# Optimization experiments

Measured on AMD Instinct MI355X. Metric: run time of the kernel, lower is better.

## Reference

```python
import jax, jax.numpy as jnp
import numpy as np

C = 512
G = 32  # num_norm_groups
EPS = 1e-6


def setup_inputs() -> dict:
    key = jax.random.key(0)
    ks = jax.random.split(key, 10)
    B, H, W = 8, 64, 64
    s = 1.0 / np.sqrt(C)
    return {
        "x": jax.random.normal(ks[0], (B, C, H, W), dtype=jnp.float32),
        "gamma": jnp.ones((C,), jnp.float32),
        "beta": jnp.zeros((C,), jnp.float32),
        "Wq": jax.random.uniform(ks[1], (C, C), jnp.float32, -s, s),
        "bq": jax.random.uniform(ks[2], (C,), jnp.float32, -s, s),
        "Wk": jax.random.uniform(ks[3], (C, C), jnp.float32, -s, s),
        "bk": jax.random.uniform(ks[4], (C,), jnp.float32, -s, s),
        "Wv": jax.random.uniform(ks[5], (C, C), jnp.float32, -s, s),
        "bv": jax.random.uniform(ks[6], (C,), jnp.float32, -s, s),
        "Wo": jax.random.uniform(ks[7], (C, C), jnp.float32, -s, s),
    }


def group_norm(x, gamma, beta):
    # x: [B, C, H, W]; normalize over each group of C//G channels and all spatial dims
    B, Cc, H, W = x.shape
    xg = x.reshape(B, G, Cc // G, H, W)
    mean = jnp.mean(xg, axis=(2, 3, 4), keepdims=True)
    var = jnp.var(xg, axis=(2, 3, 4), keepdims=True)
    xg = (xg - mean) * jax.lax.rsqrt(var + EPS)
    x = xg.reshape(B, Cc, H, W)
    return x * gamma[None, :, None, None] + beta[None, :, None, None]


def reference(x, gamma, beta, Wq, bq, Wk, bk, Wv, bv, Wo):
    B, Cc, H, W = x.shape
    out = group_norm(x, gamma, beta)
    # [B, C, H, W] -> [B, H*W, C]
    out = out.transpose(0, 2, 3, 1).reshape(B, H * W, Cc)
    q = out @ Wq.T + bq
    k = out @ Wk.T + bk
    v = out @ Wv.T + bv
    score = jnp.einsum('bic,bjc->bij', q, k) / jnp.sqrt(jnp.float32(Cc))
    score = jax.nn.softmax(score, axis=-1)
    out = jnp.einsum('bij,bjc->bic', score, v)
    out = out @ Wo.T
    out = out.reshape(B, H, W, Cc).transpose(0, 3, 1, 2)
    return out + x
```

## Files before the change

### kernel.cpp

```cpp
#include <hip/hip_runtime.h>
#include <hip/hip_bf16.h>
#include <cstdint>
#include <cstddef>

typedef __hip_bfloat16 BF;
typedef __attribute__((ext_vector_type(8))) short bhalf8;
typedef __attribute__((ext_vector_type(4))) float floatx4;

#define NB 8
#define NC 512
#define NHW 4096
#define NG 32

__device__ __forceinline__ float b2f(short h) {
    union { unsigned u; float f; } c;
    c.u = ((unsigned)(unsigned short)h) << 16;
    return c.f;
}
__device__ __forceinline__ short f2b(float f) {
    __hip_bfloat16 h = __float2bfloat16(f);
    short s;
    __builtin_memcpy(&s, &h, 2);
    return s;
}

__device__ __forceinline__ void gload16(const BF* g, BF* l) {
    __builtin_amdgcn_global_load_lds(
        (const __attribute__((address_space(1))) void*)g,
        (__attribute__((address_space(3))) void*)l, 16, 0, 0);
}

__device__ __forceinline__ void xcd_swizzle(int& bx, int& by) {
    const int gx = gridDim.x;
    const int nwg = gx * gridDim.y;
    if ((nwg & 7) == 0) {
        const int lin = by * gx + bx;
        const int cpx = nwg >> 3;
        const int s = (lin & 7) * cpx + (lin >> 3);
        bx = s % gx;
        by = s / gx;
    }
}

__global__ __launch_bounds__(256) void f2b_convert4(const float* __restrict__ s0,
                                                    const float* __restrict__ s1,
                                                    const float* __restrict__ s2,
                                                    const float* __restrict__ s3,
                                                    BF* __restrict__ dst) {
    const int which = blockIdx.x >> 8;
    const float* src = (which == 0) ? s0 : (which == 1) ? s1 : (which == 2) ? s2 : s3;
    BF* d = dst + (long)which * (NC * NC);
    const int i = ((blockIdx.x & 255) * 256 + threadIdx.x) * 4;
    float4 v = *(const float4*)&src[i];
    d[i]     = __float2bfloat16(v.x);
    d[i + 1] = __float2bfloat16(v.y);
    d[i + 2] = __float2bfloat16(v.z);
    d[i + 3] = __float2bfloat16(v.w);
}

__global__ __launch_bounds__(256) void gn_stats(const float* __restrict__ x,
                                                float* __restrict__ stats) {
    const int bg = blockIdx.x;
    const long base = (long)bg * 65536;
    float s = 0.f, q = 0.f;
    for (int i = threadIdx.x * 4; i < 65536; i += 256 * 4) {
        float4 v4 = *(const float4*)&x[base + i];
        s += v4.x + v4.y + v4.z + v4.w;
        q += v4.x * v4.x + v4.y * v4.y + v4.z * v4.z + v4.w * v4.w;
    }
#pragma unroll
    for (int o = 32; o; o >>= 1) { s += __shfl_down(s, o); q += __shfl_down(q, o); }
    __shared__ float rs[4], rq[4];
    const int w = threadIdx.x >> 6;
    if ((threadIdx.x & 63) == 0) { rs[w] = s; rq[w] = q; }
    __syncthreads();
    if (threadIdx.x == 0) {
        s = rs[0] + rs[1] + rs[2] + rs[3];
        q = rq[0] + rq[1] + rq[2] + rq[3];
        float mean = s * (1.f / 65536.f);
        float var = q * (1.f / 65536.f) - mean * mean;
        stats[2 * bg]     = mean;
        stats[2 * bg + 1] = rsqrtf(fmaxf(var, 0.f) + 1e-6f);
    }
}

__global__ __launch_bounds__(256) void gn_apply(const float* __restrict__ x,
                                                const float* __restrict__ gamma,
                                                const float* __restrict__ beta,
                                                const float* __restrict__ stats,
                                                BF* __restrict__ n) {
    __shared__ float tile[64][65];
    const int b = blockIdx.z, c0 = blockIdx.y * 64, s0 = blockIdx.x * 64;
    const long xbase = ((long)b * NC + c0) * NHW + s0;
#pragma unroll
    for (int i = 0; i < 16; i++) {
        int lin = i * 256 + threadIdx.x;
        int cl = lin >> 6, sl = lin & 63;
        int c = c0 + cl;
        float2 mr = ((const float2*)stats)[b * NG + (c >> 4)];
        float v = x[xbase + (long)cl * NHW + sl];
        v = (v - mr.x) * mr.y * gamma[c] + beta[c];
        tile[cl][sl] = v;
    }
    __syncthreads();
    const long nbase = ((long)b * NHW + s0) * NC + c0;
#pragma unroll
    for (int i = 0; i < 16; i++) {
        int lin = i * 256 + threadIdx.x;
        int sl = lin >> 6, cl = lin & 63;
        n[nbase + (long)sl * NC + cl] = __float2bfloat16(tile[cl][sl]);
    }
}

template <bool BIAS, bool TRANS, bool RESID>
__global__ __launch_bounds__(256, 2) void gemm128(
    const BF* __restrict__ A, long aStride,
    const BF* __restrict__ Bm, long bStride,
    BF* __restrict__ C, long cStride,
    const float* __restrict__ bias,
    const float* __restrict__ resid, float* __restrict__ outF,
    int M, int N, int K, float scale)
{
    __shared__ __align__(16) BF sA[128 * 32];
    __shared__ __align__(16) BF sB[128 * 32];
    const int tid = threadIdx.x;
    const int wave = tid >> 6, lane = tid & 63;
    int bxi = blockIdx.x, byi = blockIdx.y;
    xcd_swizzle(bxi, byi);
    const int bm = byi * 128, bn = bxi * 128;
    const BF* Ab = A + (long)blockIdx.z * aStride + (long)bm * K;
    const BF* Bb = Bm + (long)blockIdx.z * bStride + (long)bn * K;

    const int srow = wave * 32 + (lane >> 2);
    const int sk = (lane & 3) * 8;
    const BF* gA0 = Ab + (long)srow * K + sk;
    const BF* gA1 = gA0 + (long)16 * K;
    const BF* gB0 = Bb + (long)srow * K + sk;
    const BF* gB1 = gB0 + (long)16 * K;
    BF* lA0 = &sA[(wave * 32) * 32];
    BF* lA1 = &sA[(wave * 32 + 16) * 32];
    BF* lB0 = &sB[(wave * 32) * 32];
    BF* lB1 = &sB[(wave * 32 + 16) * 32];

    floatx4 acc[4][4];
#pragma unroll
    for (int i = 0; i < 4; i++)
#pragma unroll
        for (int j = 0; j < 4; j++) acc[i][j] = (floatx4){0.f, 0.f, 0.f, 0.f};

    const int wm = (wave >> 1) * 64, wn = (wave & 1) * 64;
    const int lr = lane & 15, lk = (lane >> 4) * 8;

    for (int k0 = 0; k0 < K; k0 += 32) {
        __syncthreads();
        gload16(gA0 + k0, lA0);
        gload16(gA1 + k0, lA1);
        gload16(gB0 + k0, lB0);
        gload16(gB1 + k0, lB1);
        __syncthreads();
        bhalf8 af[4], bfr[4];
#pragma unroll
        for (int i = 0; i < 4; i++)
            af[i] = *(const bhalf8*)&sA[(wm + i * 16 + lr) * 32 + lk];
#pragma unroll
        for (int i = 0; i < 4; i++)
            bfr[i] = *(const bhalf8*)&sB[(wn + i * 16 + lr) * 32 + lk];
#pragma unroll
        for (int mi = 0; mi < 4; mi++)
#pragma unroll
            for (int ni = 0; ni < 4; ni++)
                acc[mi][ni] = __builtin_amdgcn_mfma_f32_16x16x32_bf16(
                    af[mi], bfr[ni], acc[mi][ni], 0, 0, 0);
    }

    if (RESID) {
        float* Ob = outF + (long)blockIdx.z * cStride;
        const float* Xb = resid + (long)blockIdx.z * cStride;
#pragma unroll
        for (int ni = 0; ni < 4; ni++) {
            const int col = bn + wn + ni * 16 + lr;
#pragma unroll
            for (int mi = 0; mi < 4; mi++) {
                const int row0 = bm + wm + mi * 16 + (lane >> 4) * 4;
                const long a = (long)col * M + row0;
                float4 xv = *(const float4*)&Xb[a];
                float4 ov;
                ov.x = acc[mi][ni][0] * scale + xv.x;
                ov.y = acc[mi][ni][1] * scale + xv.y;
                ov.z = acc[mi][ni][2] * scale + xv.z;
                ov.w = acc[mi][ni][3] * scale + xv.w;
                *(float4*)&Ob[a] = ov;
            }
        }
        return;
    }

    BF* Cb = C + (long)blockIdx.z * cStride;
#pragma unroll
    for (int ni = 0; ni < 4; ni++) {
        const int col = bn + wn + ni * 16 + lr;
        const float bv = BIAS ? bias[col] : 0.0f;
#pragma unroll
        for (int mi = 0; mi < 4; mi++) {
            const int row0 = bm + wm + mi * 16 + (lane >> 4) * 4;
#pragma unroll
            for (int r = 0; r < 4; r++) {
                float v = acc[mi][ni][r] * scale + bv;
                if (TRANS) Cb[(long)col * M + row0 + r] = __float2bfloat16(v);
                else       Cb[(long)(row0 + r) * N + col] = __float2bfloat16(v);
            }
        }
    }
}

__global__ __launch_bounds__(256, 2) void gemm64(
    const BF* __restrict__ A, long aStride,
    const BF* __restrict__ Bm, long bStride,
    BF* __restrict__ C, long cStride,
    int N, int K, float scale)
{
    __shared__ __align__(16) BF sA[64 * 32];
    __shared__ __align__(16) BF sB[128 * 32];
    const int tid = threadIdx.x;
    const int wave = tid >> 6, lane = tid & 63;
    int bxi = blockIdx.x, byi = blockIdx.y;
    xcd_swizzle(bxi, byi);
    const int bm = byi * 64, bn = bxi * 128;
    const BF* Ab = A + (long)blockIdx.z * aStride + (long)bm * K;
    const BF* Bb = Bm + (long)blockIdx.z * bStride + (long)bn * K;

    const int rowoff = lane >> 2, sk = (lane & 3) * 8;
    const BF* gA0 = Ab + (long)(wave * 16 + rowoff) * K + sk;
    const BF* gB0 = Bb + (long)(wave * 32 + rowoff) * K + sk;
    const BF* gB1 = gB0 + (long)16 * K;
    BF* lA0 = &sA[(wave * 16) * 32];
    BF* lB0 = &sB[(wave * 32) * 32];
    BF* lB1 = &sB[(wave * 32 + 16) * 32];

    floatx4 acc[2][4];
#pragma unroll
    for (int i = 0; i < 2; i++)
#pragma unroll
        for (int j = 0; j < 4; j++) acc[i][j] = (floatx4){0.f, 0.f, 0.f, 0.f};

    const int wm = (wave >> 1) * 32, wn = (wave & 1) * 64;
    const int lr = lane & 15, lk = (lane >> 4) * 8;

    for (int k0 = 0; k0 < K; k0 += 32) {
        __syncthreads();
        gload16(gA0 + k0, lA0);
        gload16(gB0 + k0, lB0);
        gload16(gB1 + k0, lB1);
        __syncthreads();
        bhalf8 af[2], bfr[4];
#pragma unroll
        for (int i = 0; i < 2; i++)
            af[i] = *(const bhalf8*)&sA[(wm + i * 16 + lr) * 32 + lk];
#pragma unroll
        for (int i = 0; i < 4; i++)
            bfr[i] = *(const bhalf8*)&sB[(wn + i * 16 + lr) * 32 + lk];
#pragma unroll
        for (int mi = 0; mi < 2; mi++)
#pragma unroll
            for (int ni = 0; ni < 4; ni++)
                acc[mi][ni] = __builtin_amdgcn_mfma_f32_16x16x32_bf16(
                    af[mi], bfr[ni], acc[mi][ni], 0, 0, 0);
    }

    BF* Cb = C + (long)blockIdx.z * cStride;
#pragma unroll
    for (int ni = 0; ni < 4; ni++) {
        const int col = bn + wn + ni * 16 + lr;
#pragma unroll
        for (int mi = 0; mi < 2; mi++) {
            const int row0 = bm + wm + mi * 16 + (lane >> 4) * 4;
#pragma unroll
            for (int r = 0; r < 4; r++)
                Cb[(long)(row0 + r) * N + col] = __float2bfloat16(acc[mi][ni][r] * scale);
        }
    }
}

__global__ __launch_bounds__(256) void softmax4096(BF* __restrict__ S) {
    const long base = (long)blockIdx.x * 4096 + threadIdx.x * 16;
    const int tid = threadIdx.x, w = tid >> 6;
    bhalf8 u = *(bhalf8*)&S[base];
    bhalf8 u2 = *(bhalf8*)&S[base + 8];
    float v[16];
    float m = -1e30f;
#pragma unroll
    for (int j = 0; j < 8; j++) { v[j] = b2f(u[j]); v[8 + j] = b2f(u2[j]); }
#pragma unroll
    for (int j = 0; j < 16; j++) m = fmaxf(m, v[j]);
#pragma unroll
    for (int o = 32; o; o >>= 1) m = fmaxf(m, __shfl_xor(m, o));
    __shared__ float rm[4], rs[4];
    if ((tid & 63) == 0) rm[w] = m;
    __syncthreads();
    m = fmaxf(fmaxf(rm[0], rm[1]), fmaxf(rm[2], rm[3]));
    float s = 0.f;
#pragma unroll
    for (int j = 0; j < 16; j++) { v[j] = __expf(v[j] - m); s += v[j]; }
#pragma unroll
    for (int o = 32; o; o >>= 1) s += __shfl_xor(s, o);
    if ((tid & 63) == 0) rs[w] = s;
    __syncthreads();
    s = rs[0] + rs[1] + rs[2] + rs[3];
    const float inv = 1.0f / s;
#pragma unroll
    for (int j = 0; j < 8; j++) { u[j] = f2b(v[j] * inv); u2[j] = f2b(v[8 + j] * inv); }
    *(bhalf8*)&S[base] = u;
    *(bhalf8*)&S[base + 8] = u2;
}

extern "C" void kernel_launch(void* const* d_in, const int* in_sizes, int n_in,
                              void* d_out, int out_size, void* d_ws, size_t ws_size,
                              hipStream_t stream) {
    const float* x     = (const float*)d_in[0];
    const float* gamma = (const float*)d_in[1];
    const float* beta  = (const float*)d_in[2];
    const float* Wq    = (const float*)d_in[3];
    const float* bq    = (const float*)d_in[4];
    const float* Wk    = (const float*)d_in[5];
    const float* bk    = (const float*)d_in[6];
    const float* Wv    = (const float*)d_in[7];
    const float* bv    = (const float*)d_in[8];
    const float* Wo    = (const float*)d_in[9];
    float* out = (float*)d_out;

    const long ACTB = (long)NHW * NC;
    const long SB   = (long)NHW * NHW;
    const long WSZ  = (long)NC * NC;

    char* ws = (char*)d_ws;
    float* stats = (float*)ws;
    BF* wb = (BF*)(ws + 4096);
    BF* q  = wb + 4 * WSZ;
    BF* kk = q + NB * ACTB;
    BF* vT = kk + NB * ACTB;
    BF* R  = vT + NB * ACTB;
    BF* n = R;
    BF* S = R;

    const size_t base_need = 4096ull + (size_t)4 * WSZ * 2 + (size_t)3 * NB * ACTB * 2;
    long sroom = (ws_size > base_need) ? (long)((ws_size - base_need) / (SB * 2)) : 1;
    int chunk = (int)(sroom < 1 ? 1 : (sroom > NB ? NB : sroom));
    while (NB % chunk) chunk--;

    f2b_convert4<<<1024, 256, 0, stream>>>(Wq, Wk, Wv, Wo, wb);

    gn_stats<<<NB * NG, 256, 0, stream>>>(x, stats);
    gn_apply<<<dim3(NHW / 64, NC / 64, NB), 256, 0, stream>>>(x, gamma, beta, stats, n);

    gemm128<true, false, false><<<dim3(NC / 128, NHW / 128, NB), 256, 0, stream>>>(
        n, ACTB, wb + 0 * WSZ, 0, q, ACTB, bq, nullptr, nullptr, NHW, NC, NC, 1.0f);
    gemm128<true, false, false><<<dim3(NC / 128, NHW / 128, NB), 256, 0, stream>>>(
        n, ACTB, wb + 1 * WSZ, 0, kk, ACTB, bk, nullptr, nullptr, NHW, NC, NC, 1.0f);
    gemm128<true, true, false><<<dim3(NC / 128, NHW / 128, NB), 256, 0, stream>>>(
        n, ACTB, wb + 2 * WSZ, 0, vT, ACTB, bv, nullptr, nullptr, NHW, NC, NC, 1.0f);

    const float iscl = 0.044194173824159216f;
    for (int b0 = 0; b0 < NB; b0 += chunk) {
        gemm128<false, false, false><<<dim3(NHW / 128, NHW / 128, chunk), 256, 0, stream>>>(
            q + b0 * ACTB, ACTB, kk + b0 * ACTB, ACTB, S, SB, nullptr, nullptr, nullptr,
            NHW, NHW, NC, iscl);
        softmax4096<<<NHW * chunk, 256, 0, stream>>>(S);
        if (chunk >= 4)
            gemm128<false, false, false><<<dim3(NC / 128, NHW / 128, chunk), 256, 0, stream>>>(
                S, SB, vT + b0 * ACTB, ACTB, q + b0 * ACTB, ACTB, nullptr, nullptr, nullptr,
                NHW, NC, NHW, 1.0f);
        else
            gemm64<<<dim3(NC / 128, NHW / 64, chunk), 256, 0, stream>>>(
                S, SB, vT + b0 * ACTB, ACTB, q + b0 * ACTB, ACTB, NC, NHW, 1.0f);
    }

    gemm128<false, true, true><<<dim3(NC / 128, NHW / 128, NB), 256, 0, stream>>>(
        q, ACTB, wb + 3 * WSZ, 0, nullptr, ACTB, nullptr, x, out, NHW, NC, NC, 1.0f);
}
```

Measured before the change: 795.4 us.

## Add 256x256 double-buffered pipelined MFMA GEMM and use it for all large GEMMs

Introduces a 512-thread gemm256 kernel with 256x256 tiles and a 64-wide K step. It double-buffers 128KB of LDS with swizzled layout, interleaves global-to-LDS staging with MFMA quadrants, and uses explicit barriers, waitcnt and s_setprio. It replaces gemm128 for the QKV projections, the QK^T score GEMM, the PV GEMM (when chunk>=4) and the output projection with residual. The goal is more data reuse per tile and hiding load latency behind MFMA work. The cost is heavy LDS use that allows only one block per CU, fewer blocks for the small-N GEMMs, and fragile hand-written synchronisation.

```diff
diff --git a/kernel.cpp b/kernel.cpp
--- a/kernel.cpp
+++ b/kernel.cpp
@@ -29,6 +29,14 @@
         (const __attribute__((address_space(1))) void*)g,
         (__attribute__((address_space(3))) void*)l, 16, 0, 0);
 }
+
+__device__ __forceinline__ void BARRIER() {
+    asm volatile("" ::: "memory");
+    __builtin_amdgcn_s_barrier();
+    asm volatile("" ::: "memory");
+}
+#define WAITVM(N) asm volatile("s_waitcnt vmcnt(" #N ")" ::: "memory")
+#define WAITLGKM() asm volatile("s_waitcnt lgkmcnt(0)" ::: "memory")
 
 __device__ __forceinline__ void xcd_swizzle(int& bx, int& by) {
     const int gx = gridDim.x;
@@ -112,13 +120,211 @@
     }
 }
 
+#define LDA8(buf, mf, ks) (*(const bhalf8*)(sL + (buf) * 65536 + aOff + (mf) * 2048 + (ks) * 64))
+#define LDB8(buf, nf, ks) (*(const bhalf8*)(sL + (buf) * 65536 + bOff + (nf) * 2048 + (ks) * 64))
+#define QUAD(M0, N0)                                                                     \
+    {                                                                                    \
+        _Pragma("unroll") for (int mf = (M0); mf < (M0) + 4; mf++)                       \
+            _Pragma("unroll") for (int nf = (N0); nf < (N0) + 2; nf++) {                 \
+            acc[mf][nf] = __builtin_amdgcn_mfma_f32_16x16x32_bf16(                       \
+                aR[mf & 3][0], bR[nf][0], acc[mf][nf], 0, 0, 0);                         \
+            acc[mf][nf] = __builtin_amdgcn_mfma_f32_16x16x32_bf16(                       \
+                aR[mf & 3][1], bR[nf][1], acc[mf][nf], 0, 0, 0);                         \
+        }                                                                                \
+    }
+
 template <bool BIAS, bool TRANS, bool RESID>
+__global__ __launch_bounds__(512) void gemm256(
+    const BF* __restrict__ A, long aStride,
+    const BF* __restrict__ Bm, long bStride,
+    BF* __restrict__ C, long cStride,
+    const float* __restrict__ bias,
+    const float* __restrict__ resid, float* __restrict__ outF,
+    int M, int N, int K, float scale)
+{
+    __shared__ __align__(16) char sL[131072];
+    const int tid = threadIdx.x;
+    const int wave = tid >> 6, lane = tid & 63;
+    int bxi = blockIdx.x, byi = blockIdx.y;
+    xcd_swizzle(bxi, byi);
+    const int bm = byi * 256, bn = bxi * 256;
+    const BF* Ab = A + (long)blockIdx.z * aStride + (long)bm * K;
+    const BF* Bb = Bm + (long)blockIdx.z * bStride + (long)bn * K;
+
+    const int d0 = tid * 16, d1 = 8192 + tid * 16;
+    const int p0 = d0 ^ (((d0 >> 9) & 1) << 5);
+    const int p1 = d1 ^ (((d1 >> 9) & 1) << 5);
+    const int soff0 = (p0 >> 7) * K + ((p0 & 127) >> 1);
+    const int soff1 = (p1 >> 7) * K + ((p1 & 127) >> 1);
+    const int lds0 = wave * 1024;
+    const int lds1 = 8192 + wave * 1024;
+
+    const int lr = lane & 15, lk2 = (lane >> 4) * 16;
+    const int sbase = (lr * 128 + lk2) ^ (((lr >> 2) & 1) << 5);
+    const int aOff = (wave >> 2) * 16384 + sbase;
+    const int bOff = (2 + ((wave >> 1) & 1)) * 16384 + (wave & 1) * 8192 + sbase;
+
+    auto STAGE = [&](int t, int region, int dbuf) {
+        const BF* g = ((region < 2) ? (Ab + (long)region * 128 * K)
+                                    : (Bb + (long)(region - 2) * 128 * K)) + (long)t * 64;
+        char* lb = sL + dbuf * 65536 + region * 16384;
+        gload16(g + soff0, (BF*)(lb + lds0));
+        gload16(g + soff1, (BF*)(lb + lds1));
+    };
+
+    floatx4 acc[8][4];
+#pragma unroll
+    for (int i = 0; i < 8; i++)
+#pragma unroll
+        for (int j = 0; j < 4; j++) acc[i][j] = (floatx4){0.f, 0.f, 0.f, 0.f};
+
+    const int nt = K >> 6, ngrp = nt >> 1;
+
+    STAGE(0, 0, 0); STAGE(0, 1, 0); STAGE(0, 2, 0); STAGE(0, 3, 0);
+    WAITVM(4);
+    STAGE(1, 2, 1); STAGE(1, 3, 1); STAGE(1, 0, 1);
+    WAITVM(6);
+    BARRIER();
+
+    bhalf8 aR[4][2], bR[4][2];
+
+    for (int g = 0; g < ngrp; ++g) {
+        const bool st = (g < ngrp - 1);
+        const int t2 = 2 * g + 2, t3 = 2 * g + 3;
+
+#pragma unroll
+        for (int mf = 0; mf < 4; mf++) { aR[mf][0] = LDA8(0, mf, 0); aR[mf][1] = LDA8(0, mf, 1); }
+#pragma unroll
+        for (int nf = 0; nf < 2; nf++) { bR[nf][0] = LDB8(0, nf, 0); bR[nf][1] = LDB8(0, nf, 1); }
+        if (!(wave & 2)) {
+#pragma unroll
+            for (int nf = 2; nf < 4; nf++) { bR[nf][0] = LDB8(0, nf, 0); bR[nf][1] = LDB8(0, nf, 1); }
+        }
+        STAGE(2 * g + 1, 1, 1);
+        BARRIER(); WAITLGKM();
+        __builtin_amdgcn_s_setprio(1);
+        QUAD(0, 0);
+        __builtin_amdgcn_s_setprio(0);
+        BARRIER();
+
+        if (wave & 2) {
+#pragma unroll
+            for (int nf = 2; nf < 4; nf++) { bR[nf][0] = LDB8(0, nf, 0); bR[nf][1] = LDB8(0, nf, 1); }
+        }
+        if (st) STAGE(t2, 2, 0);
+        BARRIER(); WAITLGKM();
+        __builtin_amdgcn_s_setprio(1);
+        QUAD(0, 2);
+        __builtin_amdgcn_s_setprio(0);
+        BARRIER();
+
+#pragma unroll
+        for (int mf = 4; mf < 8; mf++) { aR[mf & 3][0] = LDA8(0, mf, 0); aR[mf & 3][1] = LDA8(0, mf, 1); }
+        if (st) STAGE(t2, 3, 0);
+        BARRIER(); WAITLGKM();
+        __builtin_amdgcn_s_setprio(1);
+        QUAD(4, 0);
+        __builtin_amdgcn_s_setprio(0);
+        BARRIER();
+
+        if (st) STAGE(t2, 0, 0);
+        BARRIER();
+        __builtin_amdgcn_s_setprio(1);
+        QUAD(4, 2);
+        __builtin_amdgcn_s_setprio(0);
+        if (st) { WAITVM(6); } else { WAITVM(0); }
+        BARRIER();
+
+#pragma unroll
+        for (int mf = 0; mf < 4; mf++) { aR[mf][0] = LDA8(1, mf, 0); aR[mf][1] = LDA8(1, mf, 1); }
+#pragma unroll
+        for (int nf = 0; nf < 2; nf++) { bR[nf][0] = LDB8(1, nf, 0); bR[nf][1] = LDB8(1, nf, 1); }
+        if (!(wave & 2)) {
+#pragma unroll
+            for (int nf = 2; nf < 4; nf++) { bR[nf][0] = LDB8(1, nf, 0); bR[nf][1] = LDB8(1, nf, 1); }
+        }
+        if (st) STAGE(t2, 1, 0);
+        BARRIER(); WAITLGKM();
+        __builtin_amdgcn_s_setprio(1);
+        QUAD(0, 0);
+        __builtin_amdgcn_s_setprio(0);
+        BARRIER();
+
+        if (wave & 2) {
+#pragma unroll
+            for (int nf = 2; nf < 4; nf++) { bR[nf][0] = LDB8(1, nf, 0); bR[nf][1] = LDB8(1, nf, 1); }
+        }
+        if (st) STAGE(t3, 2, 1);
+        BARRIER(); WAITLGKM();
+        __builtin_amdgcn_s_setprio(1);
+        QUAD(0, 2);
+        __builtin_amdgcn_s_setprio(0);
+        BARRIER();
+
+#pragma unroll
+        for (int mf = 4; mf < 8; mf++) { aR[mf & 3][0] = LDA8(1, mf, 0); aR[mf & 3][1] = LDA8(1, mf, 1); }
+        if (st) STAGE(t3, 3, 1);
+        BARRIER(); WAITLGKM();
+        __builtin_amdgcn_s_setprio(1);
+        QUAD(4, 0);
+        __builtin_amdgcn_s_setprio(0);
+        BARRIER();
+
+        if (st) STAGE(t3, 0, 1);
+        BARRIER();
+        __builtin_amdgcn_s_setprio(1);
+        QUAD(4, 2);
+        __builtin_amdgcn_s_setprio(0);
+        if (st) { WAITVM(6); }
+        BARRIER();
+    }
+
+    const int wm = (wave >> 2) * 128, wn = (wave & 3) * 64;
+    if (RESID) {
+        float* Ob = outF + (long)blockIdx.z * cStride;
+        const float* Xb = resid + (long)blockIdx.z * cStride;
+#pragma unroll
+        for (int nf = 0; nf < 4; nf++) {
+            const int col = bn + wn + nf * 16 + lr;
+#pragma unroll
+            for (int mf = 0; mf < 8; mf++) {
+                const int row0 = bm + wm + mf * 16 + (lane >> 4) * 4;
+                const long a = (long)col * M + row0;
+                float4 xv = *(const float4*)&Xb[a];
+                float4 ov;
+                ov.x = acc[mf][nf][0] * scale + xv.x;
+                ov.y = acc[mf][nf][1] * scale + xv.y;
+                ov.z = acc[mf][nf][2] * scale + xv.z;
+                ov.w = acc[mf][nf][3] * scale + xv.w;
+                *(float4*)&Ob[a] = ov;
+            }
+        }
+        return;
+    }
+    BF* Cb = C + (long)blockIdx.z * cStride;
+#pragma unroll
+    for (int nf = 0; nf < 4; nf++) {
+        const int col = bn + wn + nf * 16 + lr;
+        const float bv = BIAS ? bias[col] : 0.0f;
+#pragma unroll
+        for (int mf = 0; mf < 8; mf++) {
+            const int row0 = bm + wm + mf * 16 + (lane >> 4) * 4;
+#pragma unroll
+            for (int r = 0; r < 4; r++) {
+                float v = acc[mf][nf][r] * scale + bv;
+                if (TRANS) Cb[(long)col * M + row0 + r] = __float2bfloat16(v);
+                else       Cb[(long)(row0 + r) * N + col] = __float2bfloat16(v);
+            }
+        }
+    }
+}
+
+template <bool BIAS, bool TRANS>
 __global__ __launch_bounds__(256, 2) void gemm128(
     const BF* __restrict__ A, long aStride,
     const BF* __restrict__ Bm, long bStride,
     BF* __restrict__ C, long cStride,
     const float* __restrict__ bias,
-    const float* __restrict__ resid, float* __restrict__ outF,
     int M, int N, int K, float scale)
 {
     __shared__ __align__(16) BF sA[128 * 32];
@@ -171,28 +377,6 @@
             for (int ni = 0; ni < 4; ni++)
                 acc[mi][ni] = __builtin_amdgcn_mfma_f32_16x16x32_bf16(
                     af[mi], bfr[ni], acc[mi][ni], 0, 0, 0);
-    }
-
-    if (RESID) {
-        float* Ob = outF + (long)blockIdx.z * cStride;
-        const float* Xb = resid + (long)blockIdx.z * cStride;
-#pragma unroll
-        for (int ni = 0; ni < 4; ni++) {
-            const int col = bn + wn + ni * 16 + lr;
-#pragma unroll
-            for (int mi = 0; mi < 4; mi++) {
-                const int row0 = bm + wm + mi * 16 + (lane >> 4) * 4;
-                const long a = (long)col * M + row0;
-                float4 xv = *(const float4*)&Xb[a];
-                float4 ov;
-                ov.x = acc[mi][ni][0] * scale + xv.x;
-                ov.y = acc[mi][ni][1] * scale + xv.y;
-                ov.z = acc[mi][ni][2] * scale + xv.z;
-                ov.w = acc[mi][ni][3] * scale + xv.w;
-                *(float4*)&Ob[a] = ov;
-            }
-        }
-        return;
     }
 
     BF* Cb = C + (long)blockIdx.z * cStride;
@@ -352,28 +536,31 @@
     gn_stats<<<NB * NG, 256, 0, stream>>>(x, stats);
     gn_apply<<<dim3(NHW / 64, NC / 64, NB), 256, 0, stream>>>(x, gamma, beta, stats, n);
 
-    gemm128<true, false, false><<<dim3(NC / 128, NHW / 128, NB), 256, 0, stream>>>(
+    gemm256<true, false, false><<<dim3(NC / 256, NHW / 256, NB), 512, 0, stream>>>(
         n, ACTB, wb + 0 * WSZ, 0, q, ACTB, bq, nullptr, nullptr, NHW, NC, NC, 1.0f);
-    gemm128<true, false, false><<<dim3(NC / 128, NHW / 128, NB), 256, 0, stream>>>(
+    gemm256<true, false, false><<<dim3(NC / 256, NHW / 256, NB), 512, 0, stream>>>(
         n, ACTB, wb + 1 * WSZ, 0, kk, ACTB, bk, nullptr, nullptr, NHW, NC, NC, 1.0f);
-    gemm128<true, true, false><<<dim3(NC / 128, NHW / 128, NB), 256, 0, stream>>>(
+    gemm256<true, true, false><<<dim3(NC / 256, NHW / 256, NB), 512, 0, stream>>>(
         n, ACTB, wb + 2 * WSZ, 0, vT, ACTB, bv, nullptr, nullptr, NHW, NC, NC, 1.0f);
 
     const float iscl = 0.044194173824159216f;
     for (int b0 = 0; b0 < NB; b0 += chunk) {
-        gemm128<false, false, false><<<dim3(NHW / 128, NHW / 128, chunk), 256, 0, stream>>>(
+        gemm256<false, false, false><<<dim3(NHW / 256, NHW / 256, chunk), 512, 0, stream>>>(
             q + b0 * ACTB, ACTB, kk + b0 * ACTB, ACTB, S, SB, nullptr, nullptr, nullptr,
             NHW, NHW, NC, iscl);
         softmax4096<<<NHW * chunk, 256, 0, stream>>>(S);
         if (chunk >= 4)
-            gemm128<false, false, false><<<dim3(NC / 128, NHW / 128, chunk), 256, 0, stream>>>(
+            gemm256<false, false, false><<<dim3(NC / 256, NHW / 256, chunk), 512, 0, stream>>>(
                 S, SB, vT + b0 * ACTB, ACTB, q + b0 * ACTB, ACTB, nullptr, nullptr, nullptr,
                 NHW, NC, NHW, 1.0f);
+        else if (chunk == 2)
+            gemm128<false, false><<<dim3(NC / 128, NHW / 128, chunk), 256, 0, stream>>>(
+                S, SB, vT + b0 * ACTB, ACTB, q + b0 * ACTB, ACTB, nullptr, NHW, NC, NHW, 1.0f);
         else
             gemm64<<<dim3(NC / 128, NHW / 64, chunk), 256, 0, stream>>>(
                 S, SB, vT + b0 * ACTB, ACTB, q + b0 * ACTB, ACTB, NC, NHW, 1.0f);
     }
 
-    gemm128<false, true, true><<<dim3(NC / 128, NHW / 128, NB), 256, 0, stream>>>(
+    gemm256<false, true, true><<<dim3(NC / 256, NHW / 256, NB), 512, 0, stream>>>(
         q, ACTB, wb + 3 * WSZ, 0, nullptr, ACTB, nullptr, x, out, NHW, NC, NC, 1.0f);
 }
```

Measured after the change: 825.1 us. 1.04x slower.
